# Kernel tuning notes

Measured on AMD Instinct MI355X. Metric: run time of the kernel, lower is better.

The kernel has to match this reference:

```python
import jax, jax.numpy as jnp
import numpy as np

B, T, C, H = 4, 4096, 2048, 128  # batch, seq, emb_dim, head_size


def setup_inputs() -> dict:
    key = jax.random.key(0)
    k1, k2, k3, k4 = jax.random.split(key, 4)
    idx = jax.random.normal(k1, (B, T, C), dtype=jnp.float32)
    # nn.Linear weight layout: [out_features, in_features]; scale like torch init
    s = 1.0 / np.sqrt(C)
    Wq = jax.random.uniform(k2, (H, C), jnp.float32, -s, s)
    Wk = jax.random.uniform(k3, (H, C), jnp.float32, -s, s)
    Wv = jax.random.uniform(k4, (H, C), jnp.float32, -s, s)
    return {"idx": idx, "Wq": Wq, "Wk": Wk, "Wv": Wv}


def reference(idx, Wq, Wk, Wv):
    b, t, c = idx.shape
    q = jnp.einsum('btc,hc->bth', idx, Wq)  # [B,T,H]
    k = jnp.einsum('btc,hc->bth', idx, Wk)
    v = jnp.einsum('btc,hc->bth', idx, Wv)
    # NOTE: original computes keys @ queries^T and scales by emb_dim**-0.5
    scale = jnp.asarray(c, idx.dtype) ** -0.5
    wei = jnp.einsum('bih,bjh->bij', k, q) * scale  # [B,T,T]
    causal = jnp.tril(jnp.ones((t, t), dtype=bool))
    wei = jnp.where(causal, wei, -jnp.inf)
    wei = jax.nn.softmax(wei, axis=-1)
    return jnp.einsum('bij,bjh->bih', wei, v)  # [B,T,H]
```

## Files before the change

### kernel.cpp

```cpp
#include <hip/hip_runtime.h>
#include <hip/hip_bf16.h>
#include <cstdint>

#define TSEQ 4096
#define CDIM 2048
#define HDIM 128

typedef short bf8v __attribute__((ext_vector_type(8)));
typedef float f4v  __attribute__((ext_vector_type(4)));

__device__ __forceinline__ unsigned short f2b(float f) {
  union { float f; unsigned u; } v; v.f = f;
  unsigned u = v.u;
  return (unsigned short)((u + 0x7fffu + ((u >> 16) & 1u)) >> 16);
}

__device__ __forceinline__ f4v mfma16(bf8v a, bf8v b, f4v c) {
  return __builtin_amdgcn_mfma_f32_16x16x32_bf16(a, b, c, 0, 0, 0);
}

__global__ void wcat_kernel(const float* __restrict__ Wq, const float* __restrict__ Wk,
                            const float* __restrict__ Wv, unsigned short* __restrict__ Wcat) {
  int e = (blockIdx.x * 256 + threadIdx.x) * 4;
  int n = e >> 11;
  int k = e & 2047;
  const float* src;
  if (n < 128)      src = Wq + (size_t)n * CDIM + k;
  else if (n < 256) src = Wk + (size_t)(n - 128) * CDIM + k;
  else              src = Wv + (size_t)(n - 256) * CDIM + k;
  float4 f = *(const float4*)src;
  ushort4 o;
  o.x = f2b(f.x); o.y = f2b(f.y); o.z = f2b(f.z); o.w = f2b(f.w);
  *(ushort4*)(Wcat + e) = o;
}

__global__ __launch_bounds__(512, 6) void proj_gemm(const float* __restrict__ A,
                                                    const unsigned short* __restrict__ Bw,
                                                    unsigned short* __restrict__ QB,
                                                    unsigned short* __restrict__ KA,
                                                    unsigned short* __restrict__ VB) {
  __shared__ union {
    struct { unsigned short As[2][64][40]; unsigned short Bs[2][128][40]; } st;
    unsigned short Ct[64][132];
  } sm;
  const int m0 = blockIdx.x * 64;
  const int y  = blockIdx.y;
  const int n0 = y * 128;
  const int tid = threadIdx.x;
  const int lane = tid & 63;
  const int w = tid >> 6;
  const int wm = (w & 1) * 32, wn = (w >> 1) * 32;
  const int llo = lane & 15, lhi = lane >> 4;

  f4v acc[2][2];
#pragma unroll
  for (int i = 0; i < 2; ++i)
#pragma unroll
    for (int j = 0; j < 2; ++j) acc[i][j] = (f4v){0.f, 0.f, 0.f, 0.f};

  const int arow = tid >> 3, acol = (tid & 7) * 4;
  const int brow = tid >> 2, bcol = (tid & 3) * 8;
  const float* aptr = A + (size_t)(m0 + arow) * CDIM + acol;
  const unsigned short* bptr = Bw + (size_t)(n0 + brow) * CDIM + bcol;

  float4 fa = *(const float4*)(aptr);
  uint4  ub = *(const uint4*)(bptr);
  {
    ushort4 o;
    o.x = f2b(fa.x); o.y = f2b(fa.y); o.z = f2b(fa.z); o.w = f2b(fa.w);
    *(ushort4*)&sm.st.As[0][arow][acol] = o;
    *(uint4*)&sm.st.Bs[0][brow][bcol]   = ub;
  }

  for (int it = 0; it < 64; ++it) {
    const int cur = it & 1;
    __syncthreads();
    if (it < 63) {
      fa = *(const float4*)(aptr + (it + 1) * 32);
      ub = *(const uint4*)(bptr + (it + 1) * 32);
    }
    bf8v af[2], bfr[2];
    af[0]  = *(const bf8v*)&sm.st.As[cur][wm + llo][lhi * 8];
    af[1]  = *(const bf8v*)&sm.st.As[cur][wm + 16 + llo][lhi * 8];
    bfr[0] = *(const bf8v*)&sm.st.Bs[cur][wn + llo][lhi * 8];
    bfr[1] = *(const bf8v*)&sm.st.Bs[cur][wn + 16 + llo][lhi * 8];
#pragma unroll
    for (int i = 0; i < 2; ++i)
#pragma unroll
      for (int j = 0; j < 2; ++j) acc[i][j] = mfma16(af[i], bfr[j], acc[i][j]);
    if (it < 63) {
      ushort4 o;
      o.x = f2b(fa.x); o.y = f2b(fa.y); o.z = f2b(fa.z); o.w = f2b(fa.w);
      int nxt = cur ^ 1;
      *(ushort4*)&sm.st.As[nxt][arow][acol] = o;
      *(uint4*)&sm.st.Bs[nxt][brow][bcol]   = ub;
    }
  }
  __syncthreads();
#pragma unroll
  for (int i = 0; i < 2; ++i)
#pragma unroll
    for (int j = 0; j < 2; ++j)
#pragma unroll
      for (int r = 0; r < 4; ++r)
        sm.Ct[wm + i * 16 + lhi * 4 + r][wn + j * 16 + llo] = f2b(acc[i][j][r]);
  __syncthreads();
  if (y < 2) {
    unsigned short* dst = (y == 0) ? QB : KA;
    const size_t base16 = (size_t)(m0 >> 4);
#pragma unroll
    for (int p = 0; p < 2; ++p) {
      int g = p * 512 + tid;
      int t16l = g >> 8, kk = (g >> 6) & 3, ln = g & 63;
      int lo = ln & 15, hi = ln >> 4;
      bf8v v = *(const bf8v*)&sm.Ct[t16l * 16 + lo][kk * 32 + hi * 8];
      *(bf8v*)(dst + (((base16 + t16l) * 4 + kk) * 64 + ln) * 8) = v;
    }
  } else {
    const size_t base32 = (size_t)(m0 >> 5);
#pragma unroll
    for (int p = 0; p < 3; ++p) {
      int g = p * 512 + tid;
      if (g < 1152) {
        int jbl = g / 576;
        int ht  = (g % 576) >> 6;
        int ln  = g & 63;
        int lo = ln & 15, hi = ln >> 4;
        bf8v v;
        if (ht == 8) {
#pragma unroll
          for (int e = 0; e < 8; ++e) v[e] = (lo == 0) ? (short)0x3F80 : (short)0;
        } else {
#pragma unroll
          for (int e = 0; e < 8; ++e) v[e] = (short)sm.Ct[jbl * 32 + hi * 8 + e][ht * 16 + lo];
        }
        *(bf8v*)(VB + (((base32 + jbl) * 9 + ht) * 512 + (size_t)ln * 8)) = v;
      }
    }
  }
}

__global__ __launch_bounds__(512, 8) void attn5(const unsigned short* __restrict__ QB,
                                                const unsigned short* __restrict__ KA,
                                                const unsigned short* __restrict__ VB,
                                                float* __restrict__ out) {
  __shared__ union SM {
    unsigned short Ps[8][16][68];
    struct { float Om[8][16][66]; float Lm[8][16]; } mg;
  } sm;
  const int x = blockIdx.x;
  const int b = x & 3;
  const int u = x >> 2;
  const int g = u >> 6, r0 = u & 63;
  const int s = (g & 1) ? (g * 64 + 63 - r0) : (g * 64 + r0);
  const int lastjt = s >> 2;
  const int tid = threadIdx.x;
  const int w = tid >> 6, lane = tid & 63;
  const int llo = lane & 15, lhi = lane >> 4;
  const float scale = 0.022097086912079608f;

  bf8v aK[4];
  {
    const unsigned short* kp = KA + (size_t)(b * 256 + s) * 2048;
#pragma unroll
    for (int kk = 0; kk < 4; ++kk) aK[kk] = *(const bf8v*)(kp + (kk * 64 + lane) * 8);
  }

  f4v Oacc[9];
#pragma unroll
  for (int nt = 0; nt < 9; ++nt) Oacc[nt] = (f4v){0.f, 0.f, 0.f, 0.f};

  for (int jt = w; jt <= lastjt; jt += 8) {
    const unsigned short* qp = QB + (size_t)(b * 256 + jt * 4) * 2048;
#pragma unroll
    for (int ct = 0; ct < 4; ++ct) {
      f4v acc = (f4v){0.f, 0.f, 0.f, 0.f};
#pragma unroll
      for (int kk = 0; kk < 4; ++kk) {
        bf8v bq = *(const bf8v*)(qp + ((ct * 4 + kk) * 64 + lane) * 8);
        acc = mfma16(aK[kk], bq, acc);
      }
#pragma unroll
      for (int r = 0; r < 4; ++r) {
        float sv = acc[r];
        if (jt == lastjt) {
          int j = jt * 64 + ct * 16 + llo;
          int i = s * 16 + lhi * 4 + r;
          if (j > i) sv = -3.0e38f;
        }
        sm.Ps[w][lhi * 4 + r][ct * 16 + llo] = f2b(__expf(sv * scale));
      }
    }
    bf8v aP[2];
    aP[0] = *(const bf8v*)&sm.Ps[w][llo][lhi * 8];
    aP[1] = *(const bf8v*)&sm.Ps[w][llo][32 + lhi * 8];
    const unsigned short* vp = VB + (size_t)(b * 128 + jt * 2) * 4608;
#pragma unroll
    for (int nt = 0; nt < 9; ++nt) {
      f4v o = Oacc[nt];
#pragma unroll
      for (int kk = 0; kk < 2; ++kk) {
        bf8v bv = *(const bf8v*)(vp + kk * 4608 + nt * 512 + (size_t)lane * 8);
        o = mfma16(aP[kk], bv, o);
      }
      Oacc[nt] = o;
    }
  }

#pragma unroll
  for (int half = 0; half < 2; ++half) {
    __syncthreads();
#pragma unroll
    for (int nt = 0; nt < 4; ++nt)
#pragma unroll
      for (int r = 0; r < 4; ++r)
        sm.mg.Om[w][lhi * 4 + r][nt * 16 + llo] = Oacc[half * 4 + nt][r];
    if (half == 0 && llo == 0) {
#pragma unroll
      for (int r = 0; r < 4; ++r) sm.mg.Lm[w][lhi * 4 + r] = Oacc[8][r];
    }
    __syncthreads();
    {
      int row = tid >> 5, c0 = (tid & 31) * 2;
      float L = 0.f;
#pragma unroll
      for (int ww = 0; ww < 8; ++ww) L += sm.mg.Lm[ww][row];
      float inv = 1.0f / L;
      float o0 = 0.f, o1 = 0.f;
#pragma unroll
      for (int ww = 0; ww < 8; ++ww) {
        o0 += sm.mg.Om[ww][row][c0];
        o1 += sm.mg.Om[ww][row][c0 + 1];
      }
      float* op = out + (size_t)(b * TSEQ + s * 16 + row) * HDIM + half * 64 + c0;
      op[0] = o0 * inv;
      op[1] = o1 * inv;
    }
  }
}

extern "C" void kernel_launch(void* const* d_in, const int* in_sizes, int n_in,
                              void* d_out, int out_size, void* d_ws, size_t ws_size,
                              hipStream_t stream) {
  const float* idx = (const float*)d_in[0];
  const float* Wq  = (const float*)d_in[1];
  const float* Wk  = (const float*)d_in[2];
  const float* Wv  = (const float*)d_in[3];
  float* out = (float*)d_out;
  char* ws = (char*)d_ws;
  unsigned short* Wcat = (unsigned short*)ws;
  unsigned short* QB   = (unsigned short*)(ws + ((size_t)2  << 20));
  unsigned short* KA   = (unsigned short*)(ws + ((size_t)7  << 20));
  unsigned short* VB   = (unsigned short*)(ws + ((size_t)12 << 20));

  wcat_kernel<<<768, 256, 0, stream>>>(Wq, Wk, Wv, Wcat);
  proj_gemm<<<dim3(256, 3), 512, 0, stream>>>(idx, Wcat, QB, KA, VB);
  attn5<<<1024, 512, 0, stream>>>(QB, KA, VB, out);
}
```

Baseline: 347.1 us.

## Use 4-wave attention blocks with double-buffered score tiles

The attention kernel now runs with 256 threads (4 waves) per block instead of 8, so each wave handles twice as many key tiles. Each wave double-buffers its P tile in shared memory: it computes the next tile's QK^T and exp while issuing the current tile's PV MFMAs. This is meant to overlap the softmax/score work with the value matmuls and to cut the cross-wave merge traffic. In exchange each wave does more serial work, fewer waves are available to hide latency, and register and LDS pressure per wave go up.

```diff
diff --git a/kernel.cpp b/kernel.cpp
--- a/kernel.cpp
+++ b/kernel.cpp
@@ -140,13 +140,13 @@
   }
 }
 
-__global__ __launch_bounds__(512, 8) void attn5(const unsigned short* __restrict__ QB,
+__global__ __launch_bounds__(256, 4) void attn6(const unsigned short* __restrict__ QB,
                                                 const unsigned short* __restrict__ KA,
                                                 const unsigned short* __restrict__ VB,
                                                 float* __restrict__ out) {
   __shared__ union SM {
-    unsigned short Ps[8][16][68];
-    struct { float Om[8][16][66]; float Lm[8][16]; } mg;
+    unsigned short Ps[4][2][16][68];
+    struct { float Om[4][16][68]; float Lm[4][16]; } mg;
   } sm;
   const int x = blockIdx.x;
   const int b = x & 3;
@@ -170,8 +170,8 @@
 #pragma unroll
   for (int nt = 0; nt < 9; ++nt) Oacc[nt] = (f4v){0.f, 0.f, 0.f, 0.f};
 
-  for (int jt = w; jt <= lastjt; jt += 8) {
-    const unsigned short* qp = QB + (size_t)(b * 256 + jt * 4) * 2048;
+  auto computeS = [&](int jtS, int buf) {
+    const unsigned short* qp = QB + (size_t)(b * 256 + jtS * 4) * 2048;
 #pragma unroll
     for (int ct = 0; ct < 4; ++ct) {
       f4v acc = (f4v){0.f, 0.f, 0.f, 0.f};
@@ -183,28 +183,31 @@
 #pragma unroll
       for (int r = 0; r < 4; ++r) {
         float sv = acc[r];
-        if (jt == lastjt) {
-          int j = jt * 64 + ct * 16 + llo;
+        if (jtS == lastjt) {
+          int j = jtS * 64 + ct * 16 + llo;
           int i = s * 16 + lhi * 4 + r;
           if (j > i) sv = -3.0e38f;
         }
-        sm.Ps[w][lhi * 4 + r][ct * 16 + llo] = f2b(__expf(sv * scale));
-      }
-    }
-    bf8v aP[2];
-    aP[0] = *(const bf8v*)&sm.Ps[w][llo][lhi * 8];
-    aP[1] = *(const bf8v*)&sm.Ps[w][llo][32 + lhi * 8];
+        sm.Ps[w][buf][lhi * 4 + r][ct * 16 + llo] = f2b(__expf(sv * scale));
+      }
+    }
+  };
+
+  if (w <= lastjt) computeS(w, 0);
+  int buf = 0;
+  for (int jt = w; jt <= lastjt; jt += 4) {
+    bf8v aP0 = *(const bf8v*)&sm.Ps[w][buf][llo][lhi * 8];
+    bf8v aP1 = *(const bf8v*)&sm.Ps[w][buf][llo][32 + lhi * 8];
+    if (jt + 4 <= lastjt) computeS(jt + 4, buf ^ 1);
     const unsigned short* vp = VB + (size_t)(b * 128 + jt * 2) * 4608;
 #pragma unroll
     for (int nt = 0; nt < 9; ++nt) {
       f4v o = Oacc[nt];
-#pragma unroll
-      for (int kk = 0; kk < 2; ++kk) {
-        bf8v bv = *(const bf8v*)(vp + kk * 4608 + nt * 512 + (size_t)lane * 8);
-        o = mfma16(aP[kk], bv, o);
-      }
+      o = mfma16(aP0, *(const bf8v*)(vp + nt * 512 + (size_t)lane * 8), o);
+      o = mfma16(aP1, *(const bf8v*)(vp + 4608 + nt * 512 + (size_t)lane * 8), o);
       Oacc[nt] = o;
     }
+    buf ^= 1;
   }
 
 #pragma unroll
@@ -221,20 +224,16 @@
     }
     __syncthreads();
     {
-      int row = tid >> 5, c0 = (tid & 31) * 2;
-      float L = 0.f;
-#pragma unroll
-      for (int ww = 0; ww < 8; ++ww) L += sm.mg.Lm[ww][row];
+      int row = tid >> 4, c0 = (tid & 15) * 4;
+      float L = sm.mg.Lm[0][row] + sm.mg.Lm[1][row] + sm.mg.Lm[2][row] + sm.mg.Lm[3][row];
       float inv = 1.0f / L;
-      float o0 = 0.f, o1 = 0.f;
-#pragma unroll
-      for (int ww = 0; ww < 8; ++ww) {
-        o0 += sm.mg.Om[ww][row][c0];
-        o1 += sm.mg.Om[ww][row][c0 + 1];
-      }
       float* op = out + (size_t)(b * TSEQ + s * 16 + row) * HDIM + half * 64 + c0;
-      op[0] = o0 * inv;
-      op[1] = o1 * inv;
+#pragma unroll
+      for (int e = 0; e < 4; ++e) {
+        float o = sm.mg.Om[0][row][c0 + e] + sm.mg.Om[1][row][c0 + e] +
+                  sm.mg.Om[2][row][c0 + e] + sm.mg.Om[3][row][c0 + e];
+        op[e] = o * inv;
+      }
     }
   }
 }
@@ -255,5 +254,5 @@
 
   wcat_kernel<<<768, 256, 0, stream>>>(Wq, Wk, Wv, Wcat);
   proj_gemm<<<dim3(256, 3), 512, 0, stream>>>(idx, Wcat, QB, KA, VB);
-  attn5<<<1024, 512, 0, stream>>>(QB, KA, VB, out);
-}
+  attn6<<<1024, 256, 0, stream>>>(QB, KA, VB, out);
+}
```

Result: faster. 290.4 us (-16.3%).
